# Optimization experiments

Measured on AMD Instinct MI355X. Metric: run time of the kernel, lower is better.

## Reference

```python
import jax, jax.numpy as jnp
import numpy as np

N, E, H, IN, B, L, OUT = 50000, 600000, 128, 128, 256, 4, 10
BN_EPS = 1e-5


def setup_inputs() -> dict:
    key = jax.random.key(0)
    ks = jax.random.split(key, 12)
    x = jax.random.normal(ks[0], (N, IN), dtype=jnp.float32)
    edge_index = jax.random.randint(ks[1], (2, E), 0, N, dtype=jnp.int64)
    batch = jnp.sort(jax.random.randint(ks[2], (N,), 0, B, dtype=jnp.int64))
    s_in = 1.0 / np.sqrt(IN)
    s_h = 1.0 / np.sqrt(H)
    W_enc = jax.random.uniform(ks[3], (IN, H), jnp.float32, -s_in, s_in)
    b_enc = jax.random.uniform(ks[4], (H,), jnp.float32, -s_in, s_in)
    W = jax.random.uniform(ks[5], (L, H, H), jnp.float32, -s_h, s_h)
    b = jax.random.uniform(ks[6], (L, H), jnp.float32, -s_h, s_h)
    gamma = jnp.ones((L, H), jnp.float32)
    beta = jnp.zeros((L, H), jnp.float32)
    W_cls = jax.random.uniform(ks[7], (H, OUT), jnp.float32, -s_h, s_h)
    b_cls = jax.random.uniform(ks[8], (OUT,), jnp.float32, -s_h, s_h)
    return {"x": x, "edge_index": edge_index, "batch": batch,
            "W_enc": W_enc, "b_enc": b_enc, "W": W, "b": b,
            "gamma": gamma, "beta": beta, "W_cls": W_cls, "b_cls": b_cls}


def reference(x, edge_index, batch, W_enc, b_enc, W, b, gamma, beta, W_cls, b_cls):
    n = x.shape[0]
    # add self-loops (PyG GCNConv default)
    loop = jnp.arange(n, dtype=edge_index.dtype)
    row = jnp.concatenate([edge_index[0], loop])  # source nodes
    col = jnp.concatenate([edge_index[1], loop])  # target nodes
    # symmetric normalization: deg over targets, norm_e = d^-1/2[src] * d^-1/2[dst]
    deg = jax.ops.segment_sum(jnp.ones_like(col, dtype=x.dtype), col, num_segments=n)
    dinv = jnp.where(deg > 0, jax.lax.rsqrt(deg), 0.0)
    norm = dinv[row] * dinv[col]  # [E+N]

    # encoder (plain Linear since use_atom_encoder=False)
    h = x @ W_enc + b_enc

    for l in range(L):
        # GCNConv: transform, normalized scatter-add, bias
        t = h @ W[l]
        msg = norm[:, None] * t[row]               # [E+N, H] gather
        agg = jax.ops.segment_sum(msg, col, num_segments=n) + b[l]
        # BatchNorm1d (batch statistics, training-mode math)
        mean = jnp.mean(agg, axis=0)
        var = jnp.var(agg, axis=0)
        hn = (agg - mean) * jax.lax.rsqrt(var + BN_EPS) * gamma[l] + beta[l]
        h = jax.nn.relu(hn)  # dropout p=0.0 -> identity

    # global mean pool over graphs
    sums = jax.ops.segment_sum(h, batch, num_segments=B)
    counts = jax.ops.segment_sum(jnp.ones((n,), h.dtype), batch, num_segments=B)
    g = sums / jnp.maximum(counts, 1.0)[:, None]
    return g @ W_cls + b_cls
```

## Files before the change

### kernel.cpp

```cpp
#include <hip/hip_runtime.h>

#define NN 50000
#define NE 600000
#define HD 128
#define NL 4
#define NB 256
#define NO 10
#define BN_EPS 1e-5f

typedef short bf16x8 __attribute__((ext_vector_type(8)));
typedef float f32x4 __attribute__((ext_vector_type(4)));

__device__ __forceinline__ unsigned short f2bf(float f) {
    union { float f; unsigned int u; } x; x.f = f;
    unsigned int u = x.u;
    unsigned int r = (u + 0x7FFFu + ((u >> 16) & 1u)) >> 16;
    return (unsigned short)r;
}
__device__ __forceinline__ float bf2f(unsigned short s) {
    union { unsigned int u; float f; } x; x.u = ((unsigned int)s) << 16;
    return x.f;
}


__global__ void hist_kernel(const int* __restrict__ col, int* __restrict__ cnt, int e) {
    int i = blockIdx.x * blockDim.x + threadIdx.x;
    if (i < e) atomicAdd(&cnt[col[i]], 1);
}

__global__ void scan1_kernel(const int* __restrict__ cnt, int* __restrict__ outp,
                             int* __restrict__ bsums, float* __restrict__ dinv,
                             int M, int n) {
    __shared__ int s[256];
    int tid = threadIdx.x;
    int base = blockIdx.x * 1024 + tid * 4;
    int v[4];
#pragma unroll
    for (int j = 0; j < 4; ++j) {
        int idx = base + j;
        v[j] = (idx < n) ? cnt[idx] : 0;
        if (idx < n) dinv[idx] = rsqrtf((float)(v[j] + 1));
    }
    int tot = v[0] + v[1] + v[2] + v[3];
    s[tid] = tot;
    __syncthreads();
    for (int off = 1; off < 256; off <<= 1) {
        int x = (tid >= off) ? s[tid - off] : 0;
        __syncthreads();
        s[tid] += x;
        __syncthreads();
    }
    int run = (tid == 0) ? 0 : s[tid - 1];
#pragma unroll
    for (int j = 0; j < 4; ++j) {
        int idx = base + j;
        if (idx < M) outp[idx] = run;
        run += v[j];
    }
    if (tid == 255) bsums[blockIdx.x] = s[255];
}

__global__ void scan3_kernel(int* __restrict__ outp, const int* __restrict__ bsums, int M) {
    __shared__ int sb[64];
    int tid = threadIdx.x;
    int seg = blockIdx.x >> 2;
    if (tid < 64) sb[tid] = (tid < seg) ? bsums[tid] : 0;
    __syncthreads();
    if (tid < 32) sb[tid] += sb[tid + 32];
    __syncthreads();
    if (tid < 16) sb[tid] += sb[tid + 16];
    __syncthreads();
    if (tid < 8) sb[tid] += sb[tid + 8];
    __syncthreads();
    if (tid < 4) sb[tid] += sb[tid + 4];
    __syncthreads();
    if (tid < 2) sb[tid] += sb[tid + 2];
    __syncthreads();
    if (tid == 0) sb[0] += sb[1];
    __syncthreads();
    int i = blockIdx.x * 256 + tid;
    if (i < M) outp[i] += sb[0];
}

__global__ void place_kernel(const int* __restrict__ row, const int* __restrict__ col,
                             const float* __restrict__ dinv, int* __restrict__ rp,
                             int2* __restrict__ csr, int e) {
    int i = blockIdx.x * blockDim.x + threadIdx.x;
    if (i < e) {
        int r = row[i], c = col[i];
        int pos = atomicAdd(&rp[c], 1);
        csr[pos] = make_int2(r, __float_as_int(dinv[r] * dinv[c]));
    }
}

__global__ void wprep_kernel(const float* __restrict__ W_enc, const float* __restrict__ W,
                             const float* __restrict__ b_enc,
                             unsigned short* __restrict__ Wt, float* __restrict__ bb) {
    int bi = blockIdx.x;
    if (bi < 256) {
        int i = bi * 256 + threadIdx.x;
        int m = i >> 14;
        int r = (i >> 7) & 127;
        int k = i & 127;
        Wt[16384 + i] = f2bf(W[(size_t)m * 16384 + k * 128 + r]);
    } else if (bi < 320) {
        int gid = (bi - 256) * 256 + threadIdx.x;
        int i = gid & 127, o = gid >> 7;
        float s = 0.f;
#pragma unroll 8
        for (int h = 0; h < 128; ++h) s += W_enc[i * 128 + h] * W[h * 128 + o];
        Wt[o * 128 + i] = f2bf(s);
    } else if (threadIdx.x < 128) {
        int o = threadIdx.x;
        float s = 0.f;
#pragma unroll 8
        for (int h = 0; h < 128; ++h) s += b_enc[h] * W[h * 128 + o];
        bb[o] = s;
    }
}

template <int AMODE>
__global__ __launch_bounds__(256) void gemm128_mfma(const void* __restrict__ Ap,
                                                    const unsigned short* __restrict__ Wt,
                                                    const float* __restrict__ bias,
                                                    const float* __restrict__ bnp,
                                                    unsigned short* __restrict__ Cp,
                                                    int nrows) {
    int wave = threadIdx.x >> 6;
    int lane = threadIdx.x & 63;
    int r16 = lane & 15;
    int kg = lane >> 4;
    int rowBase = blockIdx.x * 64 + wave * 16;
    int row = rowBase + r16;
    bool valid = row < nrows;

    bf16x8 afr[4];
#pragma unroll
    for (int s = 0; s < 4; ++s) {
        bf16x8 tt = {};
        int c0 = s * 32 + kg * 8;
        if constexpr (AMODE == 0) {
            const float* A = (const float*)Ap;
            if (valid) {
                const float* p = &A[(size_t)row * 128 + c0];
                float4 u0 = *(const float4*)p;
                float4 u1 = *(const float4*)(p + 4);
                tt[0] = (short)f2bf(u0.x); tt[1] = (short)f2bf(u0.y);
                tt[2] = (short)f2bf(u0.z); tt[3] = (short)f2bf(u0.w);
                tt[4] = (short)f2bf(u1.x); tt[5] = (short)f2bf(u1.y);
                tt[6] = (short)f2bf(u1.z); tt[7] = (short)f2bf(u1.w);
            }
        } else {
            const unsigned short* A = (const unsigned short*)Ap;
            if (valid) {
                bf16x8 raw = *(const bf16x8*)&A[(size_t)row * 128 + c0];
                float4 s0 = *(const float4*)&bnp[c0];
                float4 s1 = *(const float4*)&bnp[c0 + 4];
                float4 h0 = *(const float4*)&bnp[128 + c0];
                float4 h1 = *(const float4*)&bnp[128 + c0 + 4];
                tt[0] = (short)f2bf(fmaxf(bf2f((unsigned short)raw[0]) * s0.x + h0.x, 0.f));
                tt[1] = (short)f2bf(fmaxf(bf2f((unsigned short)raw[1]) * s0.y + h0.y, 0.f));
                tt[2] = (short)f2bf(fmaxf(bf2f((unsigned short)raw[2]) * s0.z + h0.z, 0.f));
                tt[3] = (short)f2bf(fmaxf(bf2f((unsigned short)raw[3]) * s0.w + h0.w, 0.f));
                tt[4] = (short)f2bf(fmaxf(bf2f((unsigned short)raw[4]) * s1.x + h1.x, 0.f));
                tt[5] = (short)f2bf(fmaxf(bf2f((unsigned short)raw[5]) * s1.y + h1.y, 0.f));
                tt[6] = (short)f2bf(fmaxf(bf2f((unsigned short)raw[6]) * s1.z + h1.z, 0.f));
                tt[7] = (short)f2bf(fmaxf(bf2f((unsigned short)raw[7]) * s1.w + h1.w, 0.f));
            }
        }
        afr[s] = tt;
    }

    f32x4 acc[8];
#pragma unroll
    for (int n = 0; n < 8; ++n) acc[n] = (f32x4){0.f, 0.f, 0.f, 0.f};

#pragma unroll
    for (int n = 0; n < 8; ++n) {
        const unsigned short* wp = &Wt[(size_t)(n * 16 + r16) * 128 + kg * 8];
#pragma unroll
        for (int s = 0; s < 4; ++s) {
            bf16x8 wfr = *(const bf16x8*)&wp[s * 32];
            acc[n] = __builtin_amdgcn_mfma_f32_16x16x32_bf16(wfr, afr[s], acc[n], 0, 0, 0);
        }
    }

    if (valid) {
#pragma unroll
        for (int n = 0; n < 8; ++n) {
            int cbase = n * 16 + kg * 4;
            float4 bv = make_float4(0.f, 0.f, 0.f, 0.f);
            if (bias) bv = *(const float4*)&bias[cbase];
            ushort4 o;
            o.x = f2bf(acc[n][0] + bv.x);
            o.y = f2bf(acc[n][1] + bv.y);
            o.z = f2bf(acc[n][2] + bv.z);
            o.w = f2bf(acc[n][3] + bv.w);
            *(ushort4*)&Cp[(size_t)row * 128 + cbase] = o;
        }
    }
}

__global__ __launch_bounds__(256) void aggregate_kernel(const unsigned short* __restrict__ t,
                                                        const int* __restrict__ rp,
                                                        const int2* __restrict__ csr,
                                                        const float* __restrict__ dinv,
                                                        const float* __restrict__ bvec,
                                                        unsigned short* __restrict__ aggb, int n) {
    int wid = blockIdx.x * 4 + (threadIdx.x >> 6);
    int lane = threadIdx.x & 63;
    if (wid >= n) return;
    int c = lane * 2;
    float di = dinv[wid];
    float sw = di * di;
    unsigned int u = *(const unsigned int*)&t[(size_t)wid * 128 + c];
    float ax = sw * bf2f((unsigned short)(u & 0xffff)) + bvec[c];
    float ay = sw * bf2f((unsigned short)(u >> 16)) + bvec[c + 1];
    int e = (wid == 0) ? 0 : rp[wid - 1];
    int e1 = rp[wid];
    for (; e + 7 < e1; e += 8) {
        int2 ew[8];
        unsigned int uu[8];
#pragma unroll
        for (int j = 0; j < 8; ++j) ew[j] = csr[e + j];
#pragma unroll
        for (int j = 0; j < 8; ++j) uu[j] = *(const unsigned int*)&t[(size_t)ew[j].x * 128 + c];
#pragma unroll
        for (int j = 0; j < 8; ++j) {
            float w = __int_as_float(ew[j].y);
            ax += w * bf2f((unsigned short)(uu[j] & 0xffff));
            ay += w * bf2f((unsigned short)(uu[j] >> 16));
        }
    }
    for (; e + 3 < e1; e += 4) {
        int2 ew[4];
        unsigned int uu[4];
#pragma unroll
        for (int j = 0; j < 4; ++j) ew[j] = csr[e + j];
#pragma unroll
        for (int j = 0; j < 4; ++j) uu[j] = *(const unsigned int*)&t[(size_t)ew[j].x * 128 + c];
#pragma unroll
        for (int j = 0; j < 4; ++j) {
            float w = __int_as_float(ew[j].y);
            ax += w * bf2f((unsigned short)(uu[j] & 0xffff));
            ay += w * bf2f((unsigned short)(uu[j] >> 16));
        }
    }
    for (; e < e1; ++e) {
        int2 ew = csr[e];
        unsigned int u0 = *(const unsigned int*)&t[(size_t)ew.x * 128 + c];
        float w0 = __int_as_float(ew.y);
        ax += w0 * bf2f((unsigned short)(u0 & 0xffff));
        ay += w0 * bf2f((unsigned short)(u0 >> 16));
    }
    unsigned int o = (unsigned int)f2bf(ax) | ((unsigned int)f2bf(ay) << 16);
    *(unsigned int*)&aggb[(size_t)wid * 128 + c] = o;
}

#define BN_BLOCKS 256
__global__ __launch_bounds__(512) void bn_stats1_kernel(const unsigned short* __restrict__ aggb,
                                                        float* __restrict__ partials, int n) {
    int tid = threadIdx.x;
    int c4 = tid & 31, rs = tid >> 5;
    f32x4 s = {0.f, 0.f, 0.f, 0.f}, q = {0.f, 0.f, 0.f, 0.f};
    for (int r = blockIdx.x * 16 + rs; r < n; r += BN_BLOCKS * 16) {
        ushort4 v4 = *(const ushort4*)&aggb[(size_t)r * 128 + c4 * 4];
        f32x4 v = {bf2f(v4.x), bf2f(v4.y), bf2f(v4.z), bf2f(v4.w)};
        s += v;
        q += v * v;
    }
    __shared__ f32x4 ls[512], lq[512];
    ls[tid] = s;
    lq[tid] = q;
    __syncthreads();
    if (tid < 32) {
        f32x4 ss = ls[tid], qq = lq[tid];
#pragma unroll
        for (int j = 1; j < 16; ++j) { ss += ls[tid + 32 * j]; qq += lq[tid + 32 * j]; }
        float* pb = partials + (size_t)blockIdx.x * 256;
        *(f32x4*)&pb[tid * 4] = ss;
        *(f32x4*)&pb[128 + tid * 4] = qq;
    }
}

__global__ __launch_bounds__(256) void bn_stats2_kernel(const float* __restrict__ partials,
                                                        const float* __restrict__ gamma,
                                                        const float* __restrict__ beta,
                                                        float* __restrict__ bnp, float fn) {
    int tid = threadIdx.x;
    int col4 = tid & 63, g = tid >> 6;
    f32x4 acc = {0.f, 0.f, 0.f, 0.f};
#pragma unroll 8
    for (int bb = g; bb < BN_BLOCKS; bb += 4)
        acc += *(const f32x4*)&partials[(size_t)bb * 256 + col4 * 4];
    __shared__ f32x4 redv[256];
    __shared__ float red[256];
    redv[tid] = acc;
    __syncthreads();
    if (tid < 64) {
        f32x4 tot = redv[tid] + redv[tid + 64] + redv[tid + 128] + redv[tid + 192];
        *(f32x4*)&red[tid * 4] = tot;
    }
    __syncthreads();
    if (tid < 128) {
        float mean = red[tid] / fn;
        float var = fmaxf(red[128 + tid] / fn - mean * mean, 0.f);
        float sc = gamma[tid] * rsqrtf(var + BN_EPS);
        bnp[tid] = sc;
        bnp[128 + tid] = beta[tid] - mean * sc;
    }
}

__global__ __launch_bounds__(256) void pool_cls_kernel(const unsigned short* __restrict__ aggb,
                                                       const float* __restrict__ bnp,
                                                       const int* __restrict__ batch,
                                                       const float* __restrict__ Wc,
                                                       const float* __restrict__ bc,
                                                       float* __restrict__ out, int n) {
    int b = blockIdx.x;
    int tid = threadIdx.x;
    int lo = 0, hi = n;
    while (lo < hi) { int mid = (lo + hi) >> 1; if (batch[mid] < b) lo = mid + 1; else hi = mid; }
    int start = lo;
    hi = n;
    while (lo < hi) { int mid = (lo + hi) >> 1; if (batch[mid] <= b) lo = mid + 1; else hi = mid; }
    int end = lo;

    int c4 = tid & 31, rs = tid >> 5;
    f32x4 sc = *(const f32x4*)&bnp[c4 * 4];
    f32x4 sh = *(const f32x4*)&bnp[128 + c4 * 4];
    f32x4 acc = {0.f, 0.f, 0.f, 0.f};
    for (int r = start + rs; r < end; r += 8) {
        ushort4 v4 = *(const ushort4*)&aggb[(size_t)r * 128 + c4 * 4];
        f32x4 v = {bf2f(v4.x), bf2f(v4.y), bf2f(v4.z), bf2f(v4.w)};
        f32x4 y = v * sc + sh;
#pragma unroll
        for (int k = 0; k < 4; ++k) y[k] = fmaxf(y[k], 0.f);
        acc += y;
    }
    __shared__ f32x4 ls[256];
    __shared__ float g[128];
    ls[tid] = acc;
    __syncthreads();
    if (tid < 32) {
        f32x4 ss = ls[tid];
#pragma unroll
        for (int j = 1; j < 8; ++j) ss += ls[tid + 32 * j];
        float invc = 1.0f / fmaxf((float)(end - start), 1.0f);
#pragma unroll
        for (int k = 0; k < 4; ++k) g[tid * 4 + k] = ss[k] * invc;
    }
    __syncthreads();
    if (tid < NO) {
        float s = bc[tid];
        for (int c = 0; c < 128; ++c) s += g[c] * Wc[c * NO + tid];
        out[b * NO + tid] = s;
    }
}

extern "C" void kernel_launch(void* const* d_in, const int* in_sizes, int n_in,
                              void* d_out, int out_size, void* d_ws, size_t ws_size,
                              hipStream_t stream) {
    const float* x      = (const float*)d_in[0];
    const int*   eidx   = (const int*)d_in[1];
    const int*   batch  = (const int*)d_in[2];
    const float* W_enc  = (const float*)d_in[3];
    const float* b_enc  = (const float*)d_in[4];
    const float* W      = (const float*)d_in[5];
    const float* b      = (const float*)d_in[6];
    const float* gamma  = (const float*)d_in[7];
    const float* beta   = (const float*)d_in[8];
    const float* W_cls  = (const float*)d_in[9];
    const float* b_cls  = (const float*)d_in[10];
    float* out = (float*)d_out;

    const int* erow = eidx;
    const int* ecol = eidx + NE;

    float* dinv     = (float*)d_ws;
    float* partials = dinv + NN;
    float* bnp      = partials + BN_BLOCKS * 256;
    float* bb       = bnp + 256;
    int2*  csr      = (int2*)(bb + 128);
    unsigned short* t    = (unsigned short*)(csr + NE);
    unsigned short* aggb = t + (size_t)NN * HD;
    unsigned short* Wt   = aggb + (size_t)NN * HD;
    int* cnt      = (int*)(Wt + 5 * 16384);
    int* rp       = cnt + NN;
    int* bsums    = rp + NN + 1;

    hipMemsetAsync(cnt, 0, NN * sizeof(int), stream);

    hist_kernel<<<(NE + 255) / 256, 256, 0, stream>>>(ecol, cnt, NE);
    int M = NN + 1;
    int nscan = (M + 1023) / 1024;
    scan1_kernel<<<nscan, 256, 0, stream>>>(cnt, rp, bsums, dinv, M, NN);
    scan3_kernel<<<(M + 255) / 256, 256, 0, stream>>>(rp, bsums, M);
    place_kernel<<<(NE + 255) / 256, 256, 0, stream>>>(erow, ecol, dinv, rp, csr, NE);

    wprep_kernel<<<321, 256, 0, stream>>>(W_enc, W, b_enc, Wt, bb);

    int gemmBlocks = (NN + 63) / 64;
    gemm128_mfma<0><<<gemmBlocks, 256, 0, stream>>>(x, Wt, bb, nullptr, t, NN);

    for (int l = 0; l < NL; ++l) {
        if (l > 0)
            gemm128_mfma<2><<<gemmBlocks, 256, 0, stream>>>(
                aggb, Wt + (size_t)(l + 1) * 16384, nullptr, bnp, t, NN);
        aggregate_kernel<<<(NN + 3) / 4, 256, 0, stream>>>(t, rp, csr, dinv,
                                                           b + (size_t)l * HD, aggb, NN);
        bn_stats1_kernel<<<BN_BLOCKS, 512, 0, stream>>>(aggb, partials, NN);
        bn_stats2_kernel<<<1, 256, 0, stream>>>(partials, gamma + (size_t)l * HD,
                                                beta + (size_t)l * HD, bnp, (float)NN);
    }

    pool_cls_kernel<<<NB, 256, 0, stream>>>(aggb, bnp, batch, W_cls, b_cls, out, NN);
}
```

Baseline: 368.3 us.

## Fuse preprocessing kernels, merge BN stats passes, unroll aggregation by 16

```diff
diff --git a/kernel.cpp b/kernel.cpp
--- a/kernel.cpp
+++ b/kernel.cpp
@@ -7,6 +7,7 @@
 #define NB 256
 #define NO 10
 #define BN_EPS 1e-5f
+#define BN_BLOCKS 256
 
 typedef short bf16x8 __attribute__((ext_vector_type(8)));
 typedef float f32x4 __attribute__((ext_vector_type(4)));
@@ -22,89 +23,22 @@
     return x.f;
 }
 
-
-__global__ void hist_kernel(const int* __restrict__ col, int* __restrict__ cnt, int e) {
-    int i = blockIdx.x * blockDim.x + threadIdx.x;
-    if (i < e) atomicAdd(&cnt[col[i]], 1);
-}
-
-__global__ void scan1_kernel(const int* __restrict__ cnt, int* __restrict__ outp,
-                             int* __restrict__ bsums, float* __restrict__ dinv,
-                             int M, int n) {
-    __shared__ int s[256];
-    int tid = threadIdx.x;
-    int base = blockIdx.x * 1024 + tid * 4;
-    int v[4];
-#pragma unroll
-    for (int j = 0; j < 4; ++j) {
-        int idx = base + j;
-        v[j] = (idx < n) ? cnt[idx] : 0;
-        if (idx < n) dinv[idx] = rsqrtf((float)(v[j] + 1));
-    }
-    int tot = v[0] + v[1] + v[2] + v[3];
-    s[tid] = tot;
-    __syncthreads();
-    for (int off = 1; off < 256; off <<= 1) {
-        int x = (tid >= off) ? s[tid - off] : 0;
-        __syncthreads();
-        s[tid] += x;
-        __syncthreads();
-    }
-    int run = (tid == 0) ? 0 : s[tid - 1];
-#pragma unroll
-    for (int j = 0; j < 4; ++j) {
-        int idx = base + j;
-        if (idx < M) outp[idx] = run;
-        run += v[j];
-    }
-    if (tid == 255) bsums[blockIdx.x] = s[255];
-}
-
-__global__ void scan3_kernel(int* __restrict__ outp, const int* __restrict__ bsums, int M) {
-    __shared__ int sb[64];
-    int tid = threadIdx.x;
-    int seg = blockIdx.x >> 2;
-    if (tid < 64) sb[tid] = (tid < seg) ? bsums[tid] : 0;
-    __syncthreads();
-    if (tid < 32) sb[tid] += sb[tid + 32];
-    __syncthreads();
-    if (tid < 16) sb[tid] += sb[tid + 16];
-    __syncthreads();
-    if (tid < 8) sb[tid] += sb[tid + 8];
-    __syncthreads();
-    if (tid < 4) sb[tid] += sb[tid + 4];
-    __syncthreads();
-    if (tid < 2) sb[tid] += sb[tid + 2];
-    __syncthreads();
-    if (tid == 0) sb[0] += sb[1];
-    __syncthreads();
-    int i = blockIdx.x * 256 + tid;
-    if (i < M) outp[i] += sb[0];
-}
-
-__global__ void place_kernel(const int* __restrict__ row, const int* __restrict__ col,
-                             const float* __restrict__ dinv, int* __restrict__ rp,
-                             int2* __restrict__ csr, int e) {
-    int i = blockIdx.x * blockDim.x + threadIdx.x;
-    if (i < e) {
-        int r = row[i], c = col[i];
-        int pos = atomicAdd(&rp[c], 1);
-        csr[pos] = make_int2(r, __float_as_int(dinv[r] * dinv[c]));
-    }
-}
-
-__global__ void wprep_kernel(const float* __restrict__ W_enc, const float* __restrict__ W,
+__global__ void histw_kernel(const int* __restrict__ col, int* __restrict__ cnt,
+                             const float* __restrict__ W_enc, const float* __restrict__ W,
                              const float* __restrict__ b_enc,
-                             unsigned short* __restrict__ Wt, float* __restrict__ bb) {
+                             unsigned short* __restrict__ Wt, float* __restrict__ bb, int e) {
     int bi = blockIdx.x;
-    if (bi < 256) {
+    if (bi < 2344) {
         int i = bi * 256 + threadIdx.x;
+        if (i < e) atomicAdd(&cnt[col[i]], 1);
+    } else if (bi < 2600) {
+        int i = (bi - 2344) * 256 + threadIdx.x;
         int m = i >> 14;
         int r = (i >> 7) & 127;
         int k = i & 127;
         Wt[16384 + i] = f2bf(W[(size_t)m * 16384 + k * 128 + r]);
-    } else if (bi < 320) {
-        int gid = (bi - 256) * 256 + threadIdx.x;
+    } else if (bi < 2664) {
+        int gid = (bi - 2600) * 256 + threadIdx.x;
         int i = gid & 127, o = gid >> 7;
         float s = 0.f;
 #pragma unroll 8
@@ -116,6 +50,62 @@
 #pragma unroll 8
         for (int h = 0; h < 128; ++h) s += b_enc[h] * W[h * 128 + o];
         bb[o] = s;
+    }
+}
+
+__global__ void scan_kernel(const int* __restrict__ cnt, int* __restrict__ outp,
+                            float* __restrict__ dinv, int M, int n) {
+    __shared__ int s[256];
+    int tid = threadIdx.x;
+    int blk = blockIdx.x;
+
+    int lim = blk * 1024;
+    int acc = 0;
+    for (int i = tid; i < lim; i += 256) acc += cnt[i];
+    s[tid] = acc;
+    __syncthreads();
+#pragma unroll
+    for (int off = 128; off > 0; off >>= 1) {
+        if (tid < off) s[tid] += s[tid + off];
+        __syncthreads();
+    }
+    int pre = s[0];
+    __syncthreads();
+
+    int base = blk * 1024 + tid * 4;
+    int v[4];
+#pragma unroll
+    for (int j = 0; j < 4; ++j) {
+        int idx = base + j;
+        v[j] = (idx < n) ? cnt[idx] : 0;
+        if (idx < n) dinv[idx] = rsqrtf((float)(v[j] + 1));
+    }
+    int tot = v[0] + v[1] + v[2] + v[3];
+    s[tid] = tot;
+    __syncthreads();
+    for (int off = 1; off < 256; off <<= 1) {
+        int x = (tid >= off) ? s[tid - off] : 0;
+        __syncthreads();
+        s[tid] += x;
+        __syncthreads();
+    }
+    int run = pre + ((tid == 0) ? 0 : s[tid - 1]);
+#pragma unroll
+    for (int j = 0; j < 4; ++j) {
+        int idx = base + j;
+        if (idx < M) outp[idx] = run;
+        run += v[j];
+    }
+}
+
+__global__ void place_kernel(const int* __restrict__ row, const int* __restrict__ col,
+                             const float* __restrict__ dinv, int* __restrict__ rp,
+                             int2* __restrict__ csr, int e) {
+    int i = blockIdx.x * blockDim.x + threadIdx.x;
+    if (i < e) {
+        int r = row[i], c = col[i];
+        int pos = atomicAdd(&rp[c], 1);
+        csr[pos] = make_int2(r, __float_as_int(dinv[r] * dinv[c]));
     }
 }
 
@@ -218,6 +208,20 @@
     float ay = sw * bf2f((unsigned short)(u >> 16)) + bvec[c + 1];
     int e = (wid == 0) ? 0 : rp[wid - 1];
     int e1 = rp[wid];
+    for (; e + 15 < e1; e += 16) {
+        int2 ew[16];
+        unsigned int uu[16];
+#pragma unroll
+        for (int j = 0; j < 16; ++j) ew[j] = csr[e + j];
+#pragma unroll
+        for (int j = 0; j < 16; ++j) uu[j] = *(const unsigned int*)&t[(size_t)ew[j].x * 128 + c];
+#pragma unroll
+        for (int j = 0; j < 16; ++j) {
+            float w = __int_as_float(ew[j].y);
+            ax += w * bf2f((unsigned short)(uu[j] & 0xffff));
+            ay += w * bf2f((unsigned short)(uu[j] >> 16));
+        }
+    }
     for (; e + 7 < e1; e += 8) {
         int2 ew[8];
         unsigned int uu[8];
@@ -257,9 +261,12 @@
     *(unsigned int*)&aggb[(size_t)wid * 128 + c] = o;
 }
 
-#define BN_BLOCKS 256
-__global__ __launch_bounds__(512) void bn_stats1_kernel(const unsigned short* __restrict__ aggb,
-                                                        float* __restrict__ partials, int n) {
+__global__ __launch_bounds__(512) void bnf_kernel(const unsigned short* __restrict__ aggb,
+                                                  float* __restrict__ partials,
+                                                  int* __restrict__ counter,
+                                                  const float* __restrict__ gamma,
+                                                  const float* __restrict__ beta,
+                                                  float* __restrict__ bnp, int n) {
     int tid = threadIdx.x;
     int c4 = tid & 31, rs = tid >> 5;
     f32x4 s = {0.f, 0.f, 0.f, 0.f}, q = {0.f, 0.f, 0.f, 0.f};
@@ -270,6 +277,7 @@
         q += v * v;
     }
     __shared__ f32x4 ls[512], lq[512];
+    __shared__ int lastflag;
     ls[tid] = s;
     lq[tid] = q;
     __syncthreads();
@@ -280,34 +288,39 @@
         float* pb = partials + (size_t)blockIdx.x * 256;
         *(f32x4*)&pb[tid * 4] = ss;
         *(f32x4*)&pb[128 + tid * 4] = qq;
-    }
-}
-
-__global__ __launch_bounds__(256) void bn_stats2_kernel(const float* __restrict__ partials,
-                                                        const float* __restrict__ gamma,
-                                                        const float* __restrict__ beta,
-                                                        float* __restrict__ bnp, float fn) {
-    int tid = threadIdx.x;
+        __threadfence();
+    }
+    __syncthreads();
+    if (tid == 0) lastflag = (atomicAdd(counter, 1) == BN_BLOCKS - 1);
+    __syncthreads();
+    if (!lastflag) return;
+
+    __threadfence();
     int col4 = tid & 63, g = tid >> 6;
     f32x4 acc = {0.f, 0.f, 0.f, 0.f};
 #pragma unroll 8
-    for (int bb = g; bb < BN_BLOCKS; bb += 4)
+    for (int bb = g; bb < BN_BLOCKS; bb += 8)
         acc += *(const f32x4*)&partials[(size_t)bb * 256 + col4 * 4];
-    __shared__ f32x4 redv[256];
-    __shared__ float red[256];
+    __syncthreads();
+    f32x4* redv = ls;
+    float* red = (float*)lq;
     redv[tid] = acc;
     __syncthreads();
     if (tid < 64) {
-        f32x4 tot = redv[tid] + redv[tid + 64] + redv[tid + 128] + redv[tid + 192];
+        f32x4 tot = redv[tid];
+#pragma unroll
+        for (int j = 1; j < 8; ++j) tot += redv[tid + 64 * j];
         *(f32x4*)&red[tid * 4] = tot;
     }
     __syncthreads();
     if (tid < 128) {
+        float fn = (float)n;
         float mean = red[tid] / fn;
         float var = fmaxf(red[128 + tid] / fn - mean * mean, 0.f);
         float sc = gamma[tid] * rsqrtf(var + BN_EPS);
         bnp[tid] = sc;
         bnp[128 + tid] = beta[tid] - mean * sc;
+        if (tid == 0) *counter = 0;
     }
 }
 
@@ -386,19 +399,16 @@
     unsigned short* aggb = t + (size_t)NN * HD;
     unsigned short* Wt   = aggb + (size_t)NN * HD;
     int* cnt      = (int*)(Wt + 5 * 16384);
-    int* rp       = cnt + NN;
-    int* bsums    = rp + NN + 1;
-
-    hipMemsetAsync(cnt, 0, NN * sizeof(int), stream);
-
-    hist_kernel<<<(NE + 255) / 256, 256, 0, stream>>>(ecol, cnt, NE);
+    int* bncnt    = cnt + NN;
+    int* rp       = bncnt + 4;
+
+    hipMemsetAsync(cnt, 0, (NN + 4) * sizeof(int), stream);
+
+    histw_kernel<<<2665, 256, 0, stream>>>(ecol, cnt, W_enc, W, b_enc, Wt, bb, NE);
+
     int M = NN + 1;
-    int nscan = (M + 1023) / 1024;
-    scan1_kernel<<<nscan, 256, 0, stream>>>(cnt, rp, bsums, dinv, M, NN);
-    scan3_kernel<<<(M + 255) / 256, 256, 0, stream>>>(rp, bsums, M);
+    scan_kernel<<<(M + 1023) / 1024, 256, 0, stream>>>(cnt, rp, dinv, M, NN);
     place_kernel<<<(NE + 255) / 256, 256, 0, stream>>>(erow, ecol, dinv, rp, csr, NE);
-
-    wprep_kernel<<<321, 256, 0, stream>>>(W_enc, W, b_enc, Wt, bb);
 
     int gemmBlocks = (NN + 63) / 64;
     gemm128_mfma<0><<<gemmBlocks, 256, 0, stream>>>(x, Wt, bb, nullptr, t, NN);
@@ -409,9 +419,9 @@
                 aggb, Wt + (size_t)(l + 1) * 16384, nullptr, bnp, t, NN);
         aggregate_kernel<<<(NN + 3) / 4, 256, 0, stream>>>(t, rp, csr, dinv,
                                                            b + (size_t)l * HD, aggb, NN);
-        bn_stats1_kernel<<<BN_BLOCKS, 512, 0, stream>>>(aggb, partials, NN);
-        bn_stats2_kernel<<<1, 256, 0, stream>>>(partials, gamma + (size_t)l * HD,
-                                                beta + (size_t)l * HD, bnp, (float)NN);
+        bnf_kernel<<<BN_BLOCKS, 512, 0, stream>>>(aggb, partials, bncnt,
+                                                  gamma + (size_t)l * HD,
+                                                  beta + (size_t)l * HD, bnp, NN);
     }
 
     pool_cls_kernel<<<NB, 256, 0, stream>>>(aggb, bnp, batch, W_cls, b_cls, out, NN);
```

Result: slower. 410.5 us (+11.5%).
